# Kernel tuning notes

Measured on AMD Instinct MI355X. Metric: run time of the kernel, lower is better.

Reference implementation:

```python
import jax, jax.numpy as jnp
import numpy as np

N_NODES = 100000
N_EDGES = 1600000
IN_C = 64
OUT_C = 64


def setup_inputs() -> dict:
    key = jax.random.key(0)
    k1, k2, k3, k4, k5, k6 = jax.random.split(key, 6)
    x = jax.random.normal(k1, (N_NODES, IN_C), dtype=jnp.float32)
    column_index = jax.random.randint(k2, (N_EDGES,), 0, N_NODES, dtype=jnp.int32)
    row_index = jnp.sort(jax.random.randint(k3, (N_EDGES,), 0, N_NODES, dtype=jnp.int32))
    degrees = jax.random.uniform(k4, (N_NODES,), dtype=jnp.float32)
    # glorot (xavier_uniform) weight init, zero bias, matching reset_parameters()
    limit = np.sqrt(6.0 / (IN_C + OUT_C)).astype(np.float32)
    weight = jax.random.uniform(k5, (IN_C, OUT_C), dtype=jnp.float32, minval=-limit, maxval=limit)
    bias = jnp.zeros((OUT_C,), dtype=jnp.float32)
    return {"x": x, "weight": weight, "bias": bias, "column_index": column_index,
            "row_index": row_index, "degrees": degrees}


def reference(x, weight, bias, column_index, row_index, degrees):
    # GCN: transform then normalized neighbor aggregation (GNNAdvisor / ROF math).
    h = x @ weight                               # [N, out_c]
    gathered = h[column_index]                   # [E, out_c] gather source features
    agg = jax.ops.segment_sum(gathered, row_index, num_segments=N_NODES)  # [N, out_c]
    out = agg * degrees[:, None] + bias          # per-dst degree norm + bias
    return out
```

## Files before the change

### kernel.cpp

```cpp
#include <hip/hip_runtime.h>
#include <hip/hip_bf16.h>

#define IN_C 64
#define OUT_C 64
#define NPB 64

__global__ __launch_bounds__(256) void gcn_prep_kernel(
    const float* __restrict__ x, const float* __restrict__ w,
    __hip_bfloat16* __restrict__ h,
    const int* __restrict__ row, int* __restrict__ rowptr,
    int n_nodes, int n_edges, int gemm_blocks) {
    if ((int)blockIdx.x < gemm_blocks) {
        __shared__ float xl[NPB][IN_C];
        const int tid   = threadIdx.x;
        const int lane  = tid & 63;
        const int wv    = tid >> 6;
        const int node0 = blockIdx.x * NPB;
        const int nvalid = min(NPB, n_nodes - node0);

        float wcol[IN_C];
        #pragma unroll
        for (int k = 0; k < IN_C; ++k) wcol[k] = w[k * OUT_C + lane];

        const float4* x4 = (const float4*)(x + (size_t)node0 * IN_C);
        float4* xl4 = (float4*)&xl[0][0];
        #pragma unroll
        for (int i = tid; i < NPB * (IN_C / 4); i += 256) {
            const int n = i >> 4;
            float4 v = make_float4(0.f, 0.f, 0.f, 0.f);
            if (n < nvalid) v = x4[i];
            xl4[i] = v;
        }
        __syncthreads();

        for (int j = 0; j < 16; ++j) {
            const int n = wv * 16 + j;
            if (n >= nvalid) break;
            float a0 = 0.f, a1 = 0.f, a2 = 0.f, a3 = 0.f;
            #pragma unroll
            for (int k = 0; k < IN_C; k += 4) {
                a0 = fmaf(xl[n][k + 0], wcol[k + 0], a0);
                a1 = fmaf(xl[n][k + 1], wcol[k + 1], a1);
                a2 = fmaf(xl[n][k + 2], wcol[k + 2], a2);
                a3 = fmaf(xl[n][k + 3], wcol[k + 3], a3);
            }
            h[(size_t)(node0 + n) * OUT_C + lane] =
                __float2bfloat16((a0 + a1) + (a2 + a3));
        }
    } else {
        const int e = (blockIdx.x - gemm_blocks) * 256 + threadIdx.x;
        if (e >= n_edges) return;
        const int r     = row[e];
        const int rprev = (e == 0) ? -1 : row[e - 1];
        for (int n = rprev + 1; n <= r; ++n) rowptr[n] = e;
        if (e == n_edges - 1) {
            for (int n = r + 1; n <= n_nodes; ++n) rowptr[n] = n_edges;
        }
    }
}

#define UNPACK_ADD(v)                                   \
    do {                                                \
        acc[0] += __uint_as_float((v).x << 16);         \
        acc[1] += __uint_as_float((v).x & 0xFFFF0000u); \
        acc[2] += __uint_as_float((v).y << 16);         \
        acc[3] += __uint_as_float((v).y & 0xFFFF0000u); \
        acc[4] += __uint_as_float((v).z << 16);         \
        acc[5] += __uint_as_float((v).z & 0xFFFF0000u); \
        acc[6] += __uint_as_float((v).w << 16);         \
        acc[7] += __uint_as_float((v).w & 0xFFFF0000u); \
    } while (0)

__global__ __launch_bounds__(256) void gcn_agg_kernel(
    const uint4* __restrict__ h4, const int* __restrict__ col,
    const int* __restrict__ rowptr, const float* __restrict__ deg,
    const float4* __restrict__ bias4, float4* __restrict__ out4,
    int n_nodes) {
    const int tid  = threadIdx.x;
    const int node = blockIdx.x * 32 + (tid >> 3);
    if (node >= n_nodes) return;
    const int lo   = tid & 7;

    const int begin = rowptr[node];
    const int end   = rowptr[node + 1];
    const int last  = end - 1;

    float acc[8] = {0.f, 0.f, 0.f, 0.f, 0.f, 0.f, 0.f, 0.f};
    for (int e = begin; e < end; e += 8) {
        int c[8];
        #pragma unroll
        for (int i = 0; i < 8; ++i) c[i] = col[min(e + i, last)];
        uint4 v[8];
        #pragma unroll
        for (int i = 0; i < 8; ++i) v[i] = h4[(size_t)c[i] * 8 + lo];
        UNPACK_ADD(v[0]);
        #pragma unroll
        for (int i = 1; i < 8; ++i) {
            if (e + i <= last) UNPACK_ADD(v[i]);
        }
    }

    const float  d  = deg[node];
    const float4 b0 = bias4[lo * 2];
    const float4 b1 = bias4[lo * 2 + 1];
    float4 oa, ob;
    oa.x = fmaf(acc[0], d, b0.x);
    oa.y = fmaf(acc[1], d, b0.y);
    oa.z = fmaf(acc[2], d, b0.z);
    oa.w = fmaf(acc[3], d, b0.w);
    ob.x = fmaf(acc[4], d, b1.x);
    ob.y = fmaf(acc[5], d, b1.y);
    ob.z = fmaf(acc[6], d, b1.z);
    ob.w = fmaf(acc[7], d, b1.w);
    out4[(size_t)node * 16 + lo * 2]     = oa;
    out4[(size_t)node * 16 + lo * 2 + 1] = ob;
}

extern "C" void kernel_launch(void* const* d_in, const int* in_sizes, int n_in,
                              void* d_out, int out_size, void* d_ws, size_t ws_size,
                              hipStream_t stream) {
    const float* x    = (const float*)d_in[0];
    const float* w    = (const float*)d_in[1];
    const float* bias = (const float*)d_in[2];
    const int* col    = (const int*)d_in[3];
    const int* row    = (const int*)d_in[4];
    const float* deg  = (const float*)d_in[5];

    const int n_nodes = in_sizes[5];
    const int n_edges = in_sizes[3];

    __hip_bfloat16* h = (__hip_bfloat16*)d_ws;
    int* rowptr = (int*)((char*)d_ws +
                         (size_t)n_nodes * OUT_C * sizeof(__hip_bfloat16));

    const int gemm_blocks   = (n_nodes + NPB - 1) / NPB;
    const int rowptr_blocks = (n_edges + 255) / 256;
    gcn_prep_kernel<<<gemm_blocks + rowptr_blocks, 256, 0, stream>>>(
        x, w, h, row, rowptr, n_nodes, n_edges, gemm_blocks);

    const int agg_blocks = (n_nodes + 31) / 32;
    gcn_agg_kernel<<<agg_blocks, 256, 0, stream>>>(
        (const uint4*)h, col, rowptr, deg,
        (const float4*)bias, (float4*)d_out, n_nodes);
}
```

Before: 146.1 us.

## Compute x@W projection with bf16 MFMA instead of scalar FMA

Replaces the shared-memory scalar FMA GEMM in the prep kernel with per-wave 16x16x32 bf16 MFMA instructions. Each wave loads 16 rows of x directly into bf16 fragments and converts W to bf16 fragments, so no LDS staging or barrier is needed. Inputs are now rounded to bf16 before the multiply rather than only the output, which loosens precision. The GEMM is a small part of total time next to the gather aggregation, so any overall effect is likely limited.

```diff
diff --git a/kernel.cpp b/kernel.cpp
--- a/kernel.cpp
+++ b/kernel.cpp
@@ -3,52 +3,83 @@
 
 #define IN_C 64
 #define OUT_C 64
-#define NPB 64
+
+typedef __attribute__((ext_vector_type(8))) short bf16x8;
+typedef __attribute__((ext_vector_type(4))) float f32x4;
+
+__device__ __forceinline__ short f2bf(float f) {
+    unsigned u = __float_as_uint(f);
+    unsigned r = (u + 0x7FFFu + ((u >> 16) & 1u)) >> 16;
+    return (short)r;
+}
 
 __global__ __launch_bounds__(256) void gcn_prep_kernel(
     const float* __restrict__ x, const float* __restrict__ w,
-    __hip_bfloat16* __restrict__ h,
+    unsigned short* __restrict__ h,
     const int* __restrict__ row, int* __restrict__ rowptr,
     int n_nodes, int n_edges, int gemm_blocks) {
     if ((int)blockIdx.x < gemm_blocks) {
-        __shared__ float xl[NPB][IN_C];
-        const int tid   = threadIdx.x;
-        const int lane  = tid & 63;
-        const int wv    = tid >> 6;
-        const int node0 = blockIdx.x * NPB;
-        const int nvalid = min(NPB, n_nodes - node0);
+        const int lane  = threadIdx.x & 63;
+        const int wv    = threadIdx.x >> 6;
+        const int m     = lane & 15;
+        const int g     = lane >> 4;
+        const int node0 = ((int)blockIdx.x * 4 + wv) * 16;
+        if (node0 >= n_nodes) return;
 
-        float wcol[IN_C];
+        bf16x8 bfr[2][4];
         #pragma unroll
-        for (int k = 0; k < IN_C; ++k) wcol[k] = w[k * OUT_C + lane];
+        for (int ks = 0; ks < 2; ++ks) {
+            #pragma unroll
+            for (int nt = 0; nt < 4; ++nt) {
+                union { short s[8]; bf16x8 v; } u;
+                #pragma unroll
+                for (int j = 0; j < 8; ++j) {
+                    u.s[j] = f2bf(w[(ks * 32 + g * 8 + j) * OUT_C + nt * 16 + m]);
+                }
+                bfr[ks][nt] = u.v;
+            }
+        }
 
-        const float4* x4 = (const float4*)(x + (size_t)node0 * IN_C);
-        float4* xl4 = (float4*)&xl[0][0];
+        const int arow = min(node0 + m, n_nodes - 1);
+        const float* xr = x + (size_t)arow * IN_C;
+        bf16x8 afr[2];
         #pragma unroll
-        for (int i = tid; i < NPB * (IN_C / 4); i += 256) {
-            const int n = i >> 4;
-            float4 v = make_float4(0.f, 0.f, 0.f, 0.f);
-            if (n < nvalid) v = x4[i];
-            xl4[i] = v;
+        for (int ks = 0; ks < 2; ++ks) {
+            const float4 p0 = *(const float4*)(xr + ks * 32 + g * 8);
+            const float4 p1 = *(const float4*)(xr + ks * 32 + g * 8 + 4);
+            union { short s[8]; bf16x8 v; } u;
+            u.s[0] = f2bf(p0.x); u.s[1] = f2bf(p0.y);
+            u.s[2] = f2bf(p0.z); u.s[3] = f2bf(p0.w);
+            u.s[4] = f2bf(p1.x); u.s[5] = f2bf(p1.y);
+            u.s[6] = f2bf(p1.z); u.s[7] = f2bf(p1.w);
+            afr[ks] = u.v;
         }
-        __syncthreads();
 
-        for (int j = 0; j < 16; ++j) {
-            const int n = wv * 16 + j;
-            if (n >= nvalid) break;
-            float a0 = 0.f, a1 = 0.f, a2 = 0.f, a3 = 0.f;
+        f32x4 acc[4];
+        #pragma unroll
+        for (int nt = 0; nt < 4; ++nt) acc[nt] = (f32x4){0.f, 0.f, 0.f, 0.f};
+        #pragma unroll
+        for (int ks = 0; ks < 2; ++ks) {
             #pragma unroll
-            for (int k = 0; k < IN_C; k += 4) {
-                a0 = fmaf(xl[n][k + 0], wcol[k + 0], a0);
-                a1 = fmaf(xl[n][k + 1], wcol[k + 1], a1);
-                a2 = fmaf(xl[n][k + 2], wcol[k + 2], a2);
-                a3 = fmaf(xl[n][k + 3], wcol[k + 3], a3);
+            for (int nt = 0; nt < 4; ++nt) {
+                acc[nt] = __builtin_amdgcn_mfma_f32_16x16x32_bf16(
+                    afr[ks], bfr[ks][nt], acc[nt], 0, 0, 0);
             }
-            h[(size_t)(node0 + n) * OUT_C + lane] =
-                __float2bfloat16((a0 + a1) + (a2 + a3));
+        }
+
+        #pragma unroll
+        for (int j = 0; j < 4; ++j) {
+            const int node = node0 + g * 4 + j;
+            if (node < n_nodes) {
+                #pragma unroll
+                for (int nt = 0; nt < 4; ++nt) {
+                    h[(size_t)node * OUT_C + nt * 16 + m] =
+                        (unsigned short)f2bf(acc[nt][j]);
+                }
+            }
         }
     } else {
-        const int e = (blockIdx.x - gemm_blocks) * 256 + threadIdx.x;
+        const int e = ((int)blockIdx.x - gemm_blocks) * 256 + threadIdx.x;
         if (e >= n_edges) return;
         const int r     = row[e];
         const int rprev = (e == 0) ? -1 : row[e - 1];
@@ -129,11 +160,11 @@
     const int n_nodes = in_sizes[5];
     const int n_edges = in_sizes[3];
 
-    __hip_bfloat16* h = (__hip_bfloat16*)d_ws;
+    unsigned short* h = (unsigned short*)d_ws;
     int* rowptr = (int*)((char*)d_ws +
-                         (size_t)n_nodes * OUT_C * sizeof(__hip_bfloat16));
+                         (size_t)n_nodes * OUT_C * sizeof(unsigned short));
 
-    const int gemm_blocks   = (n_nodes + NPB - 1) / NPB;
+    const int gemm_blocks   = (n_nodes + 63) / 64;
     const int rowptr_blocks = (n_edges + 255) / 256;
     gcn_prep_kernel<<<gemm_blocks + rowptr_blocks, 256, 0, stream>>>(
         x, w, h, row, rowptr, n_nodes, n_edges, gemm_blocks);
```

Result: faster. 127.8 us (-12.6%).
